# Optimization experiments

Hardware: AMD Instinct MI355X
Metric: run time of the kernel (lower is better)

## Reference

```python
import jax, jax.numpy as jnp
import numpy as np

B = 16384
D = 4096  # d_mlp == d_hidden in this module
K = 64


def setup_inputs() -> dict:
    key = jax.random.key(0)
    k1, k2, k3, k4 = jax.random.split(key, 4)
    x = jax.random.normal(k1, (B, D), dtype=jnp.float32)
    ema_frequency_counter = jax.random.uniform(k2, (D,), dtype=jnp.float32)
    W_enc = jax.random.normal(k3, (D, D), dtype=jnp.float32)
    # W_dec initialized like the module: randn, then scaled by 0.1/(norm+2*eps-ish);
    # the exact init scaling: norm over dim=1, norm += eps(=1), then *= 0.1/(norm+eps)
    W_dec_raw = jax.random.normal(k4, (D, D), dtype=jnp.float32)
    eps = 1.0
    norm = jnp.linalg.norm(W_dec_raw, axis=1, keepdims=True) + eps
    W_dec = W_dec_raw * (0.1 / (norm + eps))
    pre_bias = jnp.zeros((D,), dtype=jnp.float32)
    latent_bias = jnp.zeros((D,), dtype=jnp.float32)
    return {
        'x': x,
        'ema_frequency_counter': ema_frequency_counter,
        'W_enc': W_enc,
        'W_dec': W_dec,
        'pre_bias': pre_bias,
        'latent_bias': latent_bias,
        'k': K,
    }


def topk_activation(acts, k):
    # torch.topk -> ReLU on values -> scatter back into zeros
    vals, idx = jax.lax.top_k(acts, k)          # [B, k]
    vals = jax.nn.relu(vals)
    rows = jnp.arange(acts.shape[0])[:, None]   # [B, 1]
    return jnp.zeros_like(acts).at[rows, idx].set(vals)


def reference(x, ema_frequency_counter, W_enc, W_dec, pre_bias, latent_bias, k):
    # method='reconstruct' path of TopKAutoEncoder.forward
    x_center = x - pre_bias                     # [B, D]
    acts = x_center @ W_enc + latent_bias       # [B, D]
    acts_top_k = topk_activation(acts, k)       # sparse (k nonzeros/row)
    x_reconstruct = acts_top_k @ W_dec + pre_bias
    return x_reconstruct
```

## Files before the change

kernel.cpp:

```cpp
#include <hip/hip_runtime.h>
#include <hip/hip_bf16.h>
#include <stdint.h>


typedef _Float16 half8 __attribute__((ext_vector_type(8)));
typedef float f32x4 __attribute__((ext_vector_type(4)));
typedef unsigned short ushort8 __attribute__((ext_vector_type(8)));

#define B_ROWS 16384
#define D_DIM  4096
#define TOPK   64
#define MARGIN 0.25f
#define NTILES (D_DIM / 32)

__device__ __forceinline__ void gload_lds16(const void* g, void* l) {
  __builtin_amdgcn_global_load_lds(
      (const __attribute__((address_space(1))) unsigned int*)g,
      (__attribute__((address_space(3))) unsigned int*)l, 16, 0, 0);
}

__device__ __forceinline__ unsigned short f2bf(float f) {
  unsigned u = __float_as_uint(f);
  unsigned r = (u + 0x7fffu + ((u >> 16) & 1u)) >> 16;
  return (unsigned short)r;
}


__global__ __launch_bounds__(256) void conv_x(
    const float* __restrict__ x, const float* __restrict__ pre_bias,
    _Float16* __restrict__ Xh) {
  size_t g = ((size_t)blockIdx.x * 256 + threadIdx.x) * 8;
  int col = (int)(g & (D_DIM - 1));
  float4 a = *(const float4*)(x + g);
  float4 b = *(const float4*)(x + g + 4);
  float4 p = *(const float4*)(pre_bias + col);
  float4 q = *(const float4*)(pre_bias + col + 4);
  half8 h;
  h[0] = (_Float16)(a.x - p.x); h[1] = (_Float16)(a.y - p.y);
  h[2] = (_Float16)(a.z - p.z); h[3] = (_Float16)(a.w - p.w);
  h[4] = (_Float16)(b.x - q.x); h[5] = (_Float16)(b.y - q.y);
  h[6] = (_Float16)(b.z - q.z); h[7] = (_Float16)(b.w - q.w);
  *(half8*)(Xh + g) = h;
}

__global__ __launch_bounds__(256) void transp_w(
    const float* __restrict__ W, _Float16* __restrict__ WhT,
    float* __restrict__ WT) {
  __shared__ float tile[64][65];
  int bx = blockIdx.x, by = blockIdx.y;
  int tx = threadIdx.x & 63, ty4 = threadIdx.x >> 6;
  #pragma unroll 4
  for (int i = 0; i < 16; ++i) {
    int r = ty4 * 16 + i;
    tile[r][tx] = W[(size_t)(by * 64 + r) * D_DIM + bx * 64 + tx];
  }
  __syncthreads();
  #pragma unroll 4
  for (int i = 0; i < 16; ++i) {
    int r = ty4 * 16 + i;
    float v = tile[tx][r];
    size_t o = (size_t)(bx * 64 + r) * D_DIM + by * 64 + tx;
    WT[o] = v;
    WhT[o] = (_Float16)v;
  }
}

__global__ __launch_bounds__(256) void conv_wd(
    const float* __restrict__ W, unsigned short* __restrict__ o) {
  size_t g = ((size_t)blockIdx.x * 256 + threadIdx.x) * 8;
  float4 a = *(const float4*)(W + g);
  float4 b = *(const float4*)(W + g + 4);
  ushort8 v;
  v[0] = f2bf(a.x); v[1] = f2bf(a.y); v[2] = f2bf(a.z); v[3] = f2bf(a.w);
  v[4] = f2bf(b.x); v[5] = f2bf(b.y); v[6] = f2bf(b.z); v[7] = f2bf(b.w);
  *(ushort8*)(o + g) = v;
}


#define TILE_BODY(T, VMSTR)                                                    \
  do {                                                                         \
    asm volatile("s_waitcnt " VMSTR ::: "memory");                             \
    __builtin_amdgcn_s_barrier();                                              \
    asm volatile("" ::: "memory");                                             \
    const int tt3 = (T) + 3;                                                   \
    if (tt3 < NTILES) {                                                        \
      const int bo = (tt3 & 3) * 8192;                                         \
      const int kk = tt3 * 32;                                                 \
      gload_lds16(aSrc + kk, AsB + bo + dstL);                                 \
      gload_lds16(bSrc + kk, BsB + bo + dstL);                                 \
    }                                                                          \
    {                                                                          \
      const int ab = ((T) & 3) * 8192;                                         \
      half8 bf[4], af[4];                                                      \
      _Pragma("unroll") for (int nj = 0; nj < 4; ++nj)                         \
          bf[nj] = *(const half8*)(BsB + ab + bBase + nj * 512);               \
      _Pragma("unroll") for (int mi = 0; mi < 4; ++mi)                         \
          af[mi] = *(const half8*)(AsB + ab + aBase + mi * 512);               \
      __builtin_amdgcn_s_setprio(1);                                           \
      _Pragma("unroll") for (int mi = 0; mi < 4; ++mi)                         \
          _Pragma("unroll") for (int nj = 0; nj < 4; ++nj)                     \
          acc[mi][nj] = __builtin_amdgcn_mfma_f32_16x16x32_f16(                \
              af[mi], bf[nj], acc[mi][nj], 0, 0, 0);                           \
      __builtin_amdgcn_s_setprio(0);                                           \
    }                                                                          \
  } while (0)

__global__ __launch_bounds__(1024, 4) void gemm_f16(
    const _Float16* __restrict__ A, const _Float16* __restrict__ Bt,
    const float* __restrict__ latent_bias, _Float16* __restrict__ C) {
  extern __shared__ _Float16 ldsbuf[];
  _Float16* AsB = ldsbuf;
  _Float16* BsB = ldsbuf + 4 * 8192;

  const int tid = threadIdx.x;
  const int lane = tid & 63, wave = tid >> 6;
  const int wm = wave >> 2, wn = wave & 3;

  int bid = blockIdx.x;
  int swz = (bid & 7) * (1024 >> 3) + (bid >> 3);
  const int bmBase = (swz >> 4) * 256;
  const int bnBase = (swz & 15) * 256;

  const int s = tid ^ ((tid >> 3) & 3);
  const _Float16* aSrc = A + (size_t)(bmBase + (s >> 2)) * D_DIM + (s & 3) * 8;
  const _Float16* bSrc = Bt + (size_t)(bnBase + (s >> 2)) * D_DIM + (s & 3) * 8;
  const int dstL = tid * 8;

  const int fr = lane & 15, c4 = lane >> 4;
  const int swzc = (c4 ^ ((fr >> 1) & 3)) * 8;
  const int aBase = (wm * 64 + fr) * 32 + swzc;
  const int bBase = (wn * 64 + fr) * 32 + swzc;

  f32x4 acc[4][4];
  #pragma unroll
  for (int i = 0; i < 4; ++i)
    #pragma unroll
    for (int j = 0; j < 4; ++j) acc[i][j] = f32x4{0.f, 0.f, 0.f, 0.f};

  #pragma unroll
  for (int tt = 0; tt < 3; ++tt) {
    const int bo = tt * 8192, kk = tt * 32;
    gload_lds16(aSrc + kk, AsB + bo + dstL);
    gload_lds16(bSrc + kk, BsB + bo + dstL);
  }

  for (int t = 0; t < NTILES - 2; ++t) TILE_BODY(t, "vmcnt(4)");
  TILE_BODY(NTILES - 2, "vmcnt(2)");
  TILE_BODY(NTILES - 1, "vmcnt(0)");

  const int crow0 = bmBase + wm * 64 + c4 * 4;
  const int ccol0 = bnBase + wn * 64 + fr;
  #pragma unroll
  for (int mi = 0; mi < 4; ++mi)
    #pragma unroll
    for (int nj = 0; nj < 4; ++nj) {
      int col = ccol0 + nj * 16;
      float lb = latent_bias[col];
      #pragma unroll
      for (int r = 0; r < 4; ++r)
        C[(size_t)(crow0 + mi * 16 + r) * D_DIM + col] =
            (_Float16)(acc[mi][nj][r] + lb);
    }
}


__global__ __launch_bounds__(256) void topk_full(
    const _Float16* __restrict__ acts, const float* __restrict__ x,
    const float* __restrict__ WT, const float* __restrict__ pre_bias,
    const float* __restrict__ latent_bias, float* __restrict__ vals,
    int* __restrict__ idxs) {
  const int row = blockIdx.x;
  const int tid = threadIdx.x;
  const int lane = tid & 63, wave = tid >> 6;
  __shared__ int hist[256];
  __shared__ int suf[256];
  __shared__ int sred[8];
  __shared__ int ambL[128];
  __shared__ double exv[128];
  const _Float16* arow = acts + (size_t)row * D_DIM;
  float fv[16];
  {
    half8 h0 = *(const half8*)(arow + tid * 8);
    half8 h1 = *(const half8*)(arow + 2048 + tid * 8);
    #pragma unroll
    for (int j = 0; j < 8; ++j) {
      fv[j] = (float)h0[j];
      fv[8 + j] = (float)h1[j];
    }
  }
  hist[tid] = 0;
  __syncthreads();
  #pragma unroll
  for (int e = 0; e < 16; ++e) {
    int b = (int)((fv[e] + 512.0f) * 0.25f);
    b = b < 0 ? 0 : (b > 255 ? 255 : b);
    atomicAdd(&hist[b], 1);
  }
  __syncthreads();
  int c = hist[tid];
  int sfx = c;
  #pragma unroll
  for (int off = 1; off < 64; off <<= 1) {
    int y = __shfl_down(sfx, off);
    if (lane + off < 64) sfx += y;
  }
  if (lane == 0) sred[wave] = sfx;
  __syncthreads();
  {
    int after = 0;
    for (int w = wave + 1; w < 4; ++w) after += sred[w];
    sfx += after;
  }
  suf[tid] = sfx;
  int cnd = (sfx >= TOPK) ? tid : -1;
  #pragma unroll
  for (int off = 32; off; off >>= 1) {
    int y = __shfl_down(cnd, off);
    cnd = y > cnd ? y : cnd;
  }
  if (lane == 0) sred[4 + wave] = cnd;
  __syncthreads();
  int cb;
  {
    int m0 = sred[4] > sred[5] ? sred[4] : sred[5];
    int m1 = sred[6] > sred[7] ? sred[6] : sred[7];
    cb = m0 > m1 ? m0 : m1;
  }
  const int S_above = (cb < 255) ? suf[cb + 1] : 0;
  const int rrank = TOPK - S_above;
  const float Clo = cb * 4.0f - 512.0f;
  __syncthreads();
  hist[tid] = 0;
  __syncthreads();
  #pragma unroll
  for (int e = 0; e < 16; ++e) {
    int bc = (int)((fv[e] + 512.0f) * 0.25f);
    bc = bc < 0 ? 0 : (bc > 255 ? 255 : bc);
    if (bc == cb) {
      int fb = (int)((fv[e] - Clo) * 64.0f);
      fb = fb < 0 ? 0 : (fb > 255 ? 255 : fb);
      atomicAdd(&hist[fb], 1);
    }
  }
  __syncthreads();
  int cf = hist[tid];
  int sfx2 = cf;
  #pragma unroll
  for (int off = 1; off < 64; off <<= 1) {
    int y = __shfl_down(sfx2, off);
    if (lane + off < 64) sfx2 += y;
  }
  if (lane == 0) sred[wave] = sfx2;
  __syncthreads();
  {
    int after = 0;
    for (int w = wave + 1; w < 4; ++w) after += sred[w];
    sfx2 += after;
  }
  int cnd2 = (sfx2 >= rrank) ? tid : -1;
  #pragma unroll
  for (int off = 32; off; off >>= 1) {
    int y = __shfl_down(cnd2, off);
    cnd2 = y > cnd2 ? y : cnd2;
  }
  if (lane == 0) sred[4 + wave] = cnd2;
  __syncthreads();
  int fb;
  {
    int m0 = sred[4] > sred[5] ? sred[4] : sred[5];
    int m1 = sred[6] > sred[7] ? sred[6] : sred[7];
    fb = m0 > m1 ? m0 : m1;
  }
  const float Tlo = (cb == 0 && fb == 0) ? -1e30f : (Clo + fb * 0.015625f);
  const float Thi =
      (cb == 255 && fb == 255) ? 1e30f : (Clo + (fb + 1) * 0.015625f);
  const float vhi = Thi + MARGIN;
  const float vlo = Tlo - MARGIN;
  int mC = 0, aC = 0;
  #pragma unroll
  for (int i = 0; i < 16; ++i) {
    float v = fv[i];
    if (v > vhi) ++mC;
    else if (v >= vlo) ++aC;
  }
  int xs = mC | (aC << 16);
  #pragma unroll
  for (int off = 1; off < 64; off <<= 1) {
    int y = __shfl_up(xs, off);
    if (lane >= off) xs += y;
  }
  __syncthreads();
  if (lane == 63) sred[wave] = xs;
  __syncthreads();
  int base = 0;
  for (int w = 0; w < 4; ++w)
    if (w < wave) base += sred[w];
  int tot = sred[0] + sred[1] + sred[2] + sred[3];
  int incl = base + xs;
  int mp = (incl & 0xffff) - mC;
  int ap = (incl >> 16) - aC;
  int mTot = tot & 0xffff, aTot = tot >> 16;
  const int need = TOPK - mTot;
  const bool fast = (aTot == need);
  #pragma unroll
  for (int e = 0; e < 16; ++e) {
    float v = fv[e];
    int d = (e < 8) ? (tid * 8 + e) : (2048 + tid * 8 + (e - 8));
    if (v > vhi) {
      vals[(size_t)row * TOPK + mp] = fmaxf(v, 0.0f);
      idxs[(size_t)row * TOPK + mp] = d;
      ++mp;
    } else if (v >= vlo) {
      if (fast) {
        vals[(size_t)row * TOPK + mTot + ap] = fmaxf(v, 0.0f);
        idxs[(size_t)row * TOPK + mTot + ap] = d;
      } else if (ap < 128) {
        ambL[ap] = d;
      }
      ++ap;
    }
  }
  if (fast) return;
  __syncthreads();
  const int sN = aTot > 128 ? 128 : aTot;
  const float* xr = x + (size_t)row * D_DIM;
  for (int cc = wave; cc < sN; cc += 4) {
    int d = ambL[cc];
    const float* wrow = WT + (size_t)d * D_DIM;
    double acc = 0.0;
    #pragma unroll 4
    for (int t = 0; t < 16; ++t) {
      int k0 = t * 256 + lane * 4;
      float4 xv = *(const float4*)(xr + k0);
      float4 pv = *(const float4*)(pre_bias + k0);
      float4 wv = *(const float4*)(wrow + k0);
      acc = fma((double)xv.x - (double)pv.x, (double)wv.x, acc);
      acc = fma((double)xv.y - (double)pv.y, (double)wv.y, acc);
      acc = fma((double)xv.z - (double)pv.z, (double)wv.z, acc);
      acc = fma((double)xv.w - (double)pv.w, (double)wv.w, acc);
    }
    #pragma unroll
    for (int off = 32; off; off >>= 1) acc += __shfl_down(acc, off);
    if (lane == 0) exv[cc] = acc + (double)latent_bias[d];
  }
  __syncthreads();
  if (tid == 0) {
    for (int t = 0; t < need; ++t) {
      double best = -1.0e300; int besti = 1 << 30; int bestc = -1;
      for (int cc = 0; cc < sN; ++cc) {
        double v = exv[cc];
        int d = ambL[cc];
        if (v > best || (v == best && d < besti)) {
          best = v; besti = d; bestc = cc;
        }
      }
      vals[(size_t)row * TOPK + mTot + t] = fmaxf((float)best, 0.0f);
      idxs[(size_t)row * TOPK + mTot + t] = besti;
      exv[bestc] = -1.0e300;
    }
  }
}


__global__ __launch_bounds__(256) void reconstruct(
    const unsigned short* __restrict__ Wd, const float* __restrict__ vals,
    const int* __restrict__ idxs, const float* __restrict__ pre_bias,
    float* __restrict__ out) {
  const int bid = blockIdx.x;
  const int cb = bid & 7, rowblk = bid >> 3;
  const int tid = threadIdx.x, lane = tid & 63, wave = tid >> 6;
  const int row = rowblk * 4 + wave;
  const int col0 = cb * 512 + lane * 8;
  __shared__ float sval[256];
  __shared__ int sidx[256];
  sval[tid] = vals[(size_t)(rowblk * 4 + (tid >> 6)) * TOPK + (tid & 63)];
  sidx[tid] = idxs[(size_t)(rowblk * 4 + (tid >> 6)) * TOPK + (tid & 63)];
  __syncthreads();
  float acc[8];
  float4 p0 = *(const float4*)(pre_bias + col0);
  float4 p1 = *(const float4*)(pre_bias + col0 + 4);
  acc[0] = p0.x; acc[1] = p0.y; acc[2] = p0.z; acc[3] = p0.w;
  acc[4] = p1.x; acc[5] = p1.y; acc[6] = p1.z; acc[7] = p1.w;
  #pragma unroll 4
  for (int k = 0; k < TOPK; ++k) {
    float v = sval[wave * 64 + k];
    int d = sidx[wave * 64 + k];
    ushort8 w = *(const ushort8*)(Wd + (size_t)d * D_DIM + col0);
    #pragma unroll
    for (int j = 0; j < 8; ++j)
      acc[j] = fmaf(v, __uint_as_float(((unsigned)w[j]) << 16), acc[j]);
  }
  float4 o0 = {acc[0], acc[1], acc[2], acc[3]};
  float4 o1 = {acc[4], acc[5], acc[6], acc[7]};
  *(float4*)(out + (size_t)row * D_DIM + col0) = o0;
  *(float4*)(out + (size_t)row * D_DIM + col0 + 4) = o1;
}


extern "C" void kernel_launch(void* const* d_in, const int* in_sizes, int n_in,
                              void* d_out, int out_size, void* d_ws,
                              size_t ws_size, hipStream_t stream) {
  const float* x           = (const float*)d_in[0];
  const float* W_enc       = (const float*)d_in[2];
  const float* W_dec       = (const float*)d_in[3];
  const float* pre_bias    = (const float*)d_in[4];
  const float* latent_bias = (const float*)d_in[5];
  float* out = (float*)d_out;
  _Float16* actsH = (_Float16*)d_out;
  char* ws = (char*)d_ws;
  size_t off = 0;
  auto alloc = [&](size_t bytes) {
    size_t o = off;
    off = (off + bytes + 255) & ~(size_t)255;
    return o;
  };
  _Float16* Xh        = (_Float16*)(ws + alloc((size_t)B_ROWS * D_DIM * 2));
  _Float16* WhT       = (_Float16*)(ws + alloc((size_t)D_DIM * D_DIM * 2));
  float* WT           = (float*)(ws + alloc((size_t)D_DIM * D_DIM * 4));
  unsigned short* Wd  = (unsigned short*)(ws + alloc((size_t)D_DIM * D_DIM * 2));
  float* vals         = (float*)(ws + alloc((size_t)B_ROWS * TOPK * 4));
  int* idxs           = (int*)(ws + alloc((size_t)B_ROWS * TOPK * 4));
  (void)ws_size; (void)in_sizes; (void)n_in; (void)out_size;

  (void)hipFuncSetAttribute((const void*)gemm_f16,
                            hipFuncAttributeMaxDynamicSharedMemorySize,
                            131072);

  conv_x<<<(B_ROWS * D_DIM / 8) / 256, 256, 0, stream>>>(x, pre_bias, Xh);
  transp_w<<<dim3(D_DIM / 64, D_DIM / 64), 256, 0, stream>>>(W_enc, WhT, WT);
  conv_wd<<<((size_t)D_DIM * D_DIM / 8) / 256, 256, 0, stream>>>(W_dec, Wd);
  gemm_f16<<<(B_ROWS / 256) * (D_DIM / 256), 1024, 131072, stream>>>(
      Xh, WhT, latent_bias, actsH);
  topk_full<<<B_ROWS, 256, 0, stream>>>(actsH, x, WT, pre_bias, latent_bias,
                                        vals, idxs);
  reconstruct<<<(B_ROWS / 4) * 8, 256, 0, stream>>>(Wd, vals, idxs, pre_bias,
                                                    out);
}
```

Before: 1.100 ms.

## Merge preprocessing kernels and switch GEMM to double-buffered 64-wide K stages

Merges the three preprocessing kernels (x conversion, W_enc transpose, W_dec bf16 conversion) into one launch that dispatches on block index, removing two kernel launches and their tail gaps. The GEMM main loop changes from a 4-deep ring of 32-wide K tiles with one barrier per tile to a 2-deep double buffer of 64-wide K tiles with one barrier per stage. This halves the barrier count but waits for all outstanding loads at every stage, which may expose more memory latency.

```diff
diff --git a/kernel.cpp b/kernel.cpp
--- a/kernel.cpp
+++ b/kernel.cpp
@@ -11,7 +11,7 @@
 #define D_DIM  4096
 #define TOPK   64
 #define MARGIN 0.25f
-#define NTILES (D_DIM / 32)
+#define KT64   (D_DIM / 64)
 
 __device__ __forceinline__ void gload_lds16(const void* g, void* l) {
   __builtin_amdgcn_global_load_lds(
@@ -26,91 +26,97 @@
 }
 
 
-__global__ __launch_bounds__(256) void conv_x(
+__global__ __launch_bounds__(256) void preprocess(
     const float* __restrict__ x, const float* __restrict__ pre_bias,
-    _Float16* __restrict__ Xh) {
-  size_t g = ((size_t)blockIdx.x * 256 + threadIdx.x) * 8;
-  int col = (int)(g & (D_DIM - 1));
-  float4 a = *(const float4*)(x + g);
-  float4 b = *(const float4*)(x + g + 4);
-  float4 p = *(const float4*)(pre_bias + col);
-  float4 q = *(const float4*)(pre_bias + col + 4);
-  half8 h;
-  h[0] = (_Float16)(a.x - p.x); h[1] = (_Float16)(a.y - p.y);
-  h[2] = (_Float16)(a.z - p.z); h[3] = (_Float16)(a.w - p.w);
-  h[4] = (_Float16)(b.x - q.x); h[5] = (_Float16)(b.y - q.y);
-  h[6] = (_Float16)(b.z - q.z); h[7] = (_Float16)(b.w - q.w);
-  *(half8*)(Xh + g) = h;
-}
-
-__global__ __launch_bounds__(256) void transp_w(
-    const float* __restrict__ W, _Float16* __restrict__ WhT,
-    float* __restrict__ WT) {
+    const float* __restrict__ W_enc, const float* __restrict__ W_dec,
+    _Float16* __restrict__ Xh, _Float16* __restrict__ WhT,
+    float* __restrict__ WT, unsigned short* __restrict__ Wd) {
   __shared__ float tile[64][65];
-  int bx = blockIdx.x, by = blockIdx.y;
-  int tx = threadIdx.x & 63, ty4 = threadIdx.x >> 6;
-  #pragma unroll 4
-  for (int i = 0; i < 16; ++i) {
-    int r = ty4 * 16 + i;
-    tile[r][tx] = W[(size_t)(by * 64 + r) * D_DIM + bx * 64 + tx];
-  }
-  __syncthreads();
-  #pragma unroll 4
-  for (int i = 0; i < 16; ++i) {
-    int r = ty4 * 16 + i;
-    float v = tile[tx][r];
-    size_t o = (size_t)(bx * 64 + r) * D_DIM + by * 64 + tx;
-    WT[o] = v;
-    WhT[o] = (_Float16)v;
-  }
-}
-
-__global__ __launch_bounds__(256) void conv_wd(
-    const float* __restrict__ W, unsigned short* __restrict__ o) {
-  size_t g = ((size_t)blockIdx.x * 256 + threadIdx.x) * 8;
-  float4 a = *(const float4*)(W + g);
-  float4 b = *(const float4*)(W + g + 4);
-  ushort8 v;
-  v[0] = f2bf(a.x); v[1] = f2bf(a.y); v[2] = f2bf(a.z); v[3] = f2bf(a.w);
-  v[4] = f2bf(b.x); v[5] = f2bf(b.y); v[6] = f2bf(b.z); v[7] = f2bf(b.w);
-  *(ushort8*)(o + g) = v;
-}
-
-
-#define TILE_BODY(T, VMSTR)                                                    \
+  const int bid = blockIdx.x;
+  const int tid = threadIdx.x;
+  if (bid < 32768) {
+    size_t g = ((size_t)bid * 256 + tid) * 8;
+    int col = (int)(g & (D_DIM - 1));
+    float4 a = *(const float4*)(x + g);
+    float4 b = *(const float4*)(x + g + 4);
+    float4 p = *(const float4*)(pre_bias + col);
+    float4 q = *(const float4*)(pre_bias + col + 4);
+    half8 h;
+    h[0] = (_Float16)(a.x - p.x); h[1] = (_Float16)(a.y - p.y);
+    h[2] = (_Float16)(a.z - p.z); h[3] = (_Float16)(a.w - p.w);
+    h[4] = (_Float16)(b.x - q.x); h[5] = (_Float16)(b.y - q.y);
+    h[6] = (_Float16)(b.z - q.z); h[7] = (_Float16)(b.w - q.w);
+    *(half8*)(Xh + g) = h;
+  } else if (bid < 36864) {
+    const int b2 = bid - 32768;
+    const int bx = b2 & 63, by = b2 >> 6;
+    const int tx = tid & 63, ty4 = tid >> 6;
+    #pragma unroll 4
+    for (int i = 0; i < 16; ++i) {
+      int r = ty4 * 16 + i;
+      tile[r][tx] = W_enc[(size_t)(by * 64 + r) * D_DIM + bx * 64 + tx];
+    }
+    __syncthreads();
+    #pragma unroll 4
+    for (int i = 0; i < 16; ++i) {
+      int r = ty4 * 16 + i;
+      float v = tile[tx][r];
+      size_t o = (size_t)(bx * 64 + r) * D_DIM + by * 64 + tx;
+      WT[o] = v;
+      WhT[o] = (_Float16)v;
+    }
+  } else {
+    size_t g = ((size_t)(bid - 36864) * 256 + tid) * 8;
+    float4 a = *(const float4*)(W_dec + g);
+    float4 b = *(const float4*)(W_dec + g + 4);
+    ushort8 v;
+    v[0] = f2bf(a.x); v[1] = f2bf(a.y); v[2] = f2bf(a.z); v[3] = f2bf(a.w);
+    v[4] = f2bf(b.x); v[5] = f2bf(b.y); v[6] = f2bf(b.z); v[7] = f2bf(b.w);
+    *(ushort8*)(Wd + g) = v;
+  }
+}
+
+
+#define STAGE64(T)                                                             \
   do {                                                                         \
-    asm volatile("s_waitcnt " VMSTR ::: "memory");                             \
+    const int bb_ = ((T) & 1) * 32768;                                         \
+    const int kk_ = (T) * 64;                                                  \
+    gload_lds16(aSrc + kk_, ldsbuf + bb_ + dstL);                              \
+    gload_lds16(aSrc + kk_ + 32, ldsbuf + bb_ + 8192 + dstL);                  \
+    gload_lds16(bSrc + kk_, ldsbuf + bb_ + 16384 + dstL);                      \
+    gload_lds16(bSrc + kk_ + 32, ldsbuf + bb_ + 24576 + dstL);                 \
+  } while (0)
+
+#define HALF_COMPUTE(T, KH)                                                    \
+  do {                                                                         \
+    const int ab_ = ((T) & 1) * 32768 + (KH) * 8192;                           \
+    half8 bf[4], af[4];                                                        \
+    _Pragma("unroll") for (int nj = 0; nj < 4; ++nj)                           \
+        bf[nj] = *(const half8*)(ldsbuf + ab_ + 16384 + bBase + nj * 512);     \
+    _Pragma("unroll") for (int mi = 0; mi < 4; ++mi)                           \
+        af[mi] = *(const half8*)(ldsbuf + ab_ + aBase + mi * 512);             \
+    __builtin_amdgcn_s_setprio(1);                                             \
+    _Pragma("unroll") for (int mi = 0; mi < 4; ++mi)                           \
+        _Pragma("unroll") for (int nj = 0; nj < 4; ++nj)                       \
+        acc[mi][nj] = __builtin_amdgcn_mfma_f32_16x16x32_f16(                  \
+            af[mi], bf[nj], acc[mi][nj], 0, 0, 0);                             \
+    __builtin_amdgcn_s_setprio(0);                                             \
+  } while (0)
+
+#define BODY64(T, DOSTAGE)                                                     \
+  do {                                                                         \
+    if (DOSTAGE) STAGE64((T) + 1);                                             \
+    HALF_COMPUTE(T, 0);                                                        \
+    HALF_COMPUTE(T, 1);                                                        \
+    asm volatile("s_waitcnt vmcnt(0)" ::: "memory");                           \
     __builtin_amdgcn_s_barrier();                                              \
     asm volatile("" ::: "memory");                                             \
-    const int tt3 = (T) + 3;                                                   \
-    if (tt3 < NTILES) {                                                        \
-      const int bo = (tt3 & 3) * 8192;                                         \
-      const int kk = tt3 * 32;                                                 \
-      gload_lds16(aSrc + kk, AsB + bo + dstL);                                 \
-      gload_lds16(bSrc + kk, BsB + bo + dstL);                                 \
-    }                                                                          \
-    {                                                                          \
-      const int ab = ((T) & 3) * 8192;                                         \
-      half8 bf[4], af[4];                                                      \
-      _Pragma("unroll") for (int nj = 0; nj < 4; ++nj)                         \
-          bf[nj] = *(const half8*)(BsB + ab + bBase + nj * 512);               \
-      _Pragma("unroll") for (int mi = 0; mi < 4; ++mi)                         \
-          af[mi] = *(const half8*)(AsB + ab + aBase + mi * 512);               \
-      __builtin_amdgcn_s_setprio(1);                                           \
-      _Pragma("unroll") for (int mi = 0; mi < 4; ++mi)                         \
-          _Pragma("unroll") for (int nj = 0; nj < 4; ++nj)                     \
-          acc[mi][nj] = __builtin_amdgcn_mfma_f32_16x16x32_f16(                \
-              af[mi], bf[nj], acc[mi][nj], 0, 0, 0);                           \
-      __builtin_amdgcn_s_setprio(0);                                           \
-    }                                                                          \
   } while (0)
 
 __global__ __launch_bounds__(1024, 4) void gemm_f16(
     const _Float16* __restrict__ A, const _Float16* __restrict__ Bt,
     const float* __restrict__ latent_bias, _Float16* __restrict__ C) {
   extern __shared__ _Float16 ldsbuf[];
-  _Float16* AsB = ldsbuf;
-  _Float16* BsB = ldsbuf + 4 * 8192;
 
   const int tid = threadIdx.x;
   const int lane = tid & 63, wave = tid >> 6;
@@ -137,16 +143,13 @@
     #pragma unroll
     for (int j = 0; j < 4; ++j) acc[i][j] = f32x4{0.f, 0.f, 0.f, 0.f};
 
-  #pragma unroll
-  for (int tt = 0; tt < 3; ++tt) {
-    const int bo = tt * 8192, kk = tt * 32;
-    gload_lds16(aSrc + kk, AsB + bo + dstL);
-    gload_lds16(bSrc + kk, BsB + bo + dstL);
-  }
-
-  for (int t = 0; t < NTILES - 2; ++t) TILE_BODY(t, "vmcnt(4)");
-  TILE_BODY(NTILES - 2, "vmcnt(2)");
-  TILE_BODY(NTILES - 1, "vmcnt(0)");
+  STAGE64(0);
+  asm volatile("s_waitcnt vmcnt(0)" ::: "memory");
+  __builtin_amdgcn_s_barrier();
+  asm volatile("" ::: "memory");
+
+  for (int t = 0; t < KT64 - 1; ++t) BODY64(t, true);
+  BODY64(KT64 - 1, false);
 
   const int crow0 = bmBase + wm * 64 + c4 * 4;
   const int ccol0 = bnBase + wn * 64 + fr;
@@ -426,9 +429,8 @@
                             hipFuncAttributeMaxDynamicSharedMemorySize,
                             131072);
 
-  conv_x<<<(B_ROWS * D_DIM / 8) / 256, 256, 0, stream>>>(x, pre_bias, Xh);
-  transp_w<<<dim3(D_DIM / 64, D_DIM / 64), 256, 0, stream>>>(W_enc, WhT, WT);
-  conv_wd<<<((size_t)D_DIM * D_DIM / 8) / 256, 256, 0, stream>>>(W_dec, Wd);
+  preprocess<<<45056, 256, 0, stream>>>(x, pre_bias, W_enc, W_dec,
+                                        Xh, WhT, WT, Wd);
   gemm_f16<<<(B_ROWS / 256) * (D_DIM / 256), 1024, 131072, stream>>>(
       Xh, WhT, latent_bias, actsH);
   topk_full<<<B_ROWS, 256, 0, stream>>>(actsH, x, WT, pre_bias, latent_bias,
```

Result: faster. 1.070 ms, median of 2 (-2.7%).
